# Kernel optimization log

Measured on AMD Instinct MI355X. Metric: run time of the kernel, lower is better.

Reference implementation:

```python
import jax, jax.numpy as jnp
import numpy as np

B, S, L, D, H, F, V = 8, 1024, 12, 768, 12, 3072, 21128
TITLE_LEN, CONTENTS_LEN = 64, 960
DH = D // H
NEG_INF = -1e9


def setup_inputs() -> dict:
    key = jax.random.key(0)
    ks = jax.random.split(key, 14)
    p = lambda k, shape: (0.02 * jax.random.normal(k, shape)).astype(jnp.float32)
    return {
        "x": jax.random.randint(ks[0], (B, S), 0, V),
        "y": jax.random.randint(ks[1], (B, CONTENTS_LEN), 0, V),
        "word_emb": p(ks[2], (V, D)),
        "pos_emb": p(ks[3], (S, D)),
        "type_emb": p(ks[4], (2, D)),
        "emb_ln_g": jnp.ones((D,), jnp.float32),
        "emb_ln_b": jnp.zeros((D,), jnp.float32),
        "Wq": p(ks[5], (L, D, D)), "bq": jnp.zeros((L, D), jnp.float32),
        "Wk": p(ks[6], (L, D, D)), "bk": jnp.zeros((L, D), jnp.float32),
        "Wv": p(ks[7], (L, D, D)), "bv": jnp.zeros((L, D), jnp.float32),
        "Wo": p(ks[8], (L, D, D)), "bo": jnp.zeros((L, D), jnp.float32),
        "ln1_g": jnp.ones((L, D), jnp.float32), "ln1_b": jnp.zeros((L, D), jnp.float32),
        "W1": p(ks[9], (L, D, F)), "b1": jnp.zeros((L, F), jnp.float32),
        "W2": p(ks[10], (L, F, D)), "b2": jnp.zeros((L, D), jnp.float32),
        "ln2_g": jnp.ones((L, D), jnp.float32), "ln2_b": jnp.zeros((L, D), jnp.float32),
        "cls_W": p(ks[11], (D, V)), "cls_b": jnp.zeros((V,), jnp.float32),
    }


def _ln(x, g, b):
    m = x.mean(-1, keepdims=True)
    v = jnp.mean((x - m) ** 2, -1, keepdims=True)
    return (x - m) * jax.lax.rsqrt(v + 1e-12) * g + b


def _forward(x, y, word_emb, pos_emb, type_emb, emb_ln_g, emb_ln_b,
             Wq, bq, Wk, bk, Wv, bv, Wo, bo, ln1_g, ln1_b,
             W1, b1, W2, b2, ln2_g, ln2_b, cls_W, cls_b):
    # prefix-LM mask: causal (tril) except fully-visible title block [S,S]
    mask = jnp.tril(jnp.ones((S, S), jnp.float32))
    mask = mask.at[:TITLE_LEN, :TITLE_LEN].set(1.0)
    bias = (1.0 - mask) * NEG_INF  # additive attention bias

    h = word_emb[x] + pos_emb[None, :, :] + type_emb[0]  # [B,S,D]
    h = _ln(h, emb_ln_g, emb_ln_b)

    scale = 1.0 / np.sqrt(DH).astype(np.float32)

    def step(h, p):
        Wq_, bq_, Wk_, bk_, Wv_, bv_, Wo_, bo_, g1, bb1, W1_, bf1, W2_, bf2, g2, bb2 = p
        q = (h @ Wq_ + bq_).reshape(B, S, H, DH)
        k = (h @ Wk_ + bk_).reshape(B, S, H, DH)
        v = (h @ Wv_ + bv_).reshape(B, S, H, DH)
        scores = jnp.einsum('bqhd,bkhd->bhqk', q, k) * scale + bias  # [B,H,S,S]
        a = jax.nn.softmax(scores, axis=-1)
        ctx = jnp.einsum('bhqk,bkhd->bqhd', a, v).reshape(B, S, D)
        h = _ln(h + ctx @ Wo_ + bo_, g1, bb1)
        ffn = jax.nn.gelu(h @ W1_ + bf1, approximate=False) @ W2_ + bf2
        h = _ln(h + ffn, g2, bb2)
        return h, None

    h, _ = jax.lax.scan(step, h, (Wq, bq, Wk, bk, Wv, bv, Wo, bo,
                                  ln1_g, ln1_b, W1, b1, W2, b2, ln2_g, ln2_b))

    logits = h[:, -CONTENTS_LEN:, :] @ cls_W + cls_b  # [B,C,V]
    logp = jax.nn.log_softmax(logits, axis=-1)
    valid = (y != -100)
    yc = jnp.where(valid, y, 0)
    nll = -jnp.take_along_axis(logp, yc[..., None], axis=-1)[..., 0]
    return jnp.sum(nll * valid) / jnp.maximum(jnp.sum(valid), 1)


def reference(x, y, word_emb, pos_emb, type_emb, emb_ln_g, emb_ln_b,
              Wq, bq, Wk, bk, Wv, bv, Wo, bo, ln1_g, ln1_b,
              W1, b1, W2, b2, ln2_g, ln2_b, cls_W, cls_b):
    return _forward(x, y, word_emb, pos_emb, type_emb, emb_ln_g, emb_ln_b,
                    Wq, bq, Wk, bk, Wv, bv, Wo, bo, ln1_g, ln1_b,
                    W1, b1, W2, b2, ln2_g, ln2_b, cls_W, cls_b)
```

## Files before the change

kernel.cpp:

```cpp
#include <hip/hip_runtime.h>

#define BB 8
#define SS 1024
#define LL 12
#define DD 768
#define HH 12
#define FF 3072
#define VV 21128
#define DH 64
#define CLEN 960
#define NROWS (BB * CLEN)
#define TOKS (BB * SS)
#define NQKV 2304
#define QKW 1536

typedef __attribute__((ext_vector_type(8))) short bh8;
typedef __attribute__((ext_vector_type(4))) float f32x4;
typedef __attribute__((ext_vector_type(4))) unsigned short us4;

__device__ __forceinline__ float bf2f(unsigned short u) {
    union { unsigned int i; float f; } c; c.i = ((unsigned int)u) << 16; return c.f;
}
__device__ __forceinline__ unsigned short f2bf(float f) {
    union { float f; unsigned int i; } c; c.f = f;
    unsigned int r = c.i + 0x7fffu + ((c.i >> 16) & 1u);
    return (unsigned short)(r >> 16);
}

#define GLOAD16(gsrc, ldst)                                                              \
    __builtin_amdgcn_global_load_lds((const __attribute__((address_space(1))) unsigned int*)(gsrc), \
                                     (__attribute__((address_space(3))) unsigned int*)(ldst), 16, 0, 0)

__device__ __forceinline__ float bsum256(float v, float* red) {
#pragma unroll
    for (int o = 32; o; o >>= 1) v += __shfl_down(v, o);
    if ((threadIdx.x & 63) == 0) red[threadIdx.x >> 6] = v;
    __syncthreads();
    float r = red[0] + red[1] + red[2] + red[3];
    __syncthreads();
    return r;
}

__global__ void transpose_f32_bf16(const float* __restrict__ in, unsigned short* __restrict__ out,
                                   int R, int C) {
    __shared__ float tile[32][33];
    int c0 = blockIdx.x << 5, r0 = blockIdx.y << 5;
    int tx = threadIdx.x, ty = threadIdx.y;
    for (int i = ty; i < 32; i += 8) {
        int r = r0 + i, c = c0 + tx;
        if (r < R && c < C) tile[i][tx] = in[(size_t)r * C + c];
    }
    __syncthreads();
    for (int i = ty; i < 32; i += 8) {
        int oc = c0 + i, orr = r0 + tx;
        if (oc < C && orr < R) out[(size_t)oc * R + orr] = f2bf(tile[tx][i]);
    }
}

__global__ void transpose_all(const float* __restrict__ Wq, const float* __restrict__ Wk,
                              const float* __restrict__ Wv, const float* __restrict__ Wo,
                              const float* __restrict__ W1, const float* __restrict__ W2,
                              unsigned short* __restrict__ wqkvT, unsigned short* __restrict__ woT,
                              unsigned short* __restrict__ w1T, unsigned short* __restrict__ w2T) {
    __shared__ float tile[32][33];
    int t0 = blockIdx.x;
    int l = t0 / 6912, t = t0 - l * 6912;
    const float* src;
    unsigned short* dst;
    int R, C, txt, tt;
    if (t < 1728) {
        int which = t / 576; tt = t % 576;
        src = (which == 0 ? Wq : (which == 1 ? Wk : Wv)) + (size_t)l * DD * DD;
        dst = wqkvT + (size_t)l * NQKV * DD + (size_t)which * DD * DD;
        R = DD; C = DD; txt = 24;
    } else if (t < 2304) {
        tt = t - 1728; src = Wo + (size_t)l * DD * DD; dst = woT + (size_t)l * DD * DD;
        R = DD; C = DD; txt = 24;
    } else if (t < 4608) {
        tt = t - 2304; src = W1 + (size_t)l * DD * FF; dst = w1T + (size_t)l * DD * FF;
        R = DD; C = FF; txt = 96;
    } else {
        tt = t - 4608; src = W2 + (size_t)l * FF * DD; dst = w2T + (size_t)l * FF * DD;
        R = FF; C = DD; txt = 24;
    }
    int c0 = (tt % txt) << 5, r0 = (tt / txt) << 5;
    int tx = threadIdx.x, ty = threadIdx.y;
    for (int i = ty; i < 32; i += 8) tile[i][tx] = src[(size_t)(r0 + i) * C + c0 + tx];
    __syncthreads();
    for (int i = ty; i < 32; i += 8) dst[(size_t)(c0 + i) * R + r0 + tx] = f2bf(tile[tx][i]);
}

__global__ void transpose_layer(const float* __restrict__ Wq, const float* __restrict__ Wk,
                                const float* __restrict__ Wv, const float* __restrict__ Wo,
                                const float* __restrict__ W1, const float* __restrict__ W2,
                                unsigned short* __restrict__ wqkvT, unsigned short* __restrict__ woT,
                                unsigned short* __restrict__ w1T, unsigned short* __restrict__ w2T) {
    __shared__ float tile[32][33];
    int t = blockIdx.x;
    const float* src;
    unsigned short* dst;
    int R, C, txt, tt;
    if (t < 1728) {
        int which = t / 576; tt = t % 576;
        src = which == 0 ? Wq : (which == 1 ? Wk : Wv);
        dst = wqkvT + (size_t)which * DD * DD; R = DD; C = DD; txt = 24;
    } else if (t < 2304) {
        tt = t - 1728; src = Wo; dst = woT; R = DD; C = DD; txt = 24;
    } else if (t < 4608) {
        tt = t - 2304; src = W1; dst = w1T; R = DD; C = FF; txt = 96;
    } else {
        tt = t - 4608; src = W2; dst = w2T; R = FF; C = DD; txt = 24;
    }
    int c0 = (tt % txt) << 5, r0 = (tt / txt) << 5;
    int tx = threadIdx.x, ty = threadIdx.y;
    for (int i = ty; i < 32; i += 8) tile[i][tx] = src[(size_t)(r0 + i) * C + c0 + tx];
    __syncthreads();
    for (int i = ty; i < 32; i += 8) dst[(size_t)(c0 + i) * R + r0 + tx] = f2bf(tile[tx][i]);
}

__global__ void concat_bias_all(const float* __restrict__ bq, const float* __restrict__ bk,
                                const float* __restrict__ bv, float* __restrict__ out) {
    int i = blockIdx.x * 256 + threadIdx.x;
    if (i >= LL * NQKV) return;
    int l = i / NQKV, c = i % NQKV;
    float v = c < DD ? bq[(size_t)l * DD + c]
                     : (c < 2 * DD ? bk[(size_t)l * DD + c - DD] : bv[(size_t)l * DD + c - 2 * DD]);
    out[i] = v;
}

__global__ __launch_bounds__(256) void embed_ln(const int* __restrict__ x, const float* __restrict__ we,
                                                const float* __restrict__ pe, const float* __restrict__ te,
                                                const float* __restrict__ g, const float* __restrict__ be,
                                                unsigned short* __restrict__ hb) {
    int row = blockIdx.x;
    int s = row & (SS - 1);
    int tok = x[row];
    int tid = threadIdx.x;
    __shared__ float red[4];
    float v[3];
#pragma unroll
    for (int i = 0; i < 3; i++) {
        int c = tid + i * 256;
        v[i] = we[(size_t)tok * DD + c] + pe[(size_t)s * DD + c] + te[c];
    }
    float mean = bsum256(v[0] + v[1] + v[2], red) * (1.f / DD);
    float d0 = v[0] - mean, d1 = v[1] - mean, d2 = v[2] - mean;
    float var = bsum256(d0 * d0 + d1 * d1 + d2 * d2, red) * (1.f / DD);
    float inv = rsqrtf(var + 1e-12f);
    size_t base = (size_t)row * DD;
#pragma unroll
    for (int i = 0; i < 3; i++) {
        int c = tid + i * 256;
        hb[base + c] = f2bf((v[i] - mean) * inv * g[c] + be[c]);
    }
}

__global__ __launch_bounds__(256) void add_ln(const unsigned short* __restrict__ res,
                                              const unsigned short* __restrict__ t,
                                              const float* __restrict__ g, const float* __restrict__ be,
                                              unsigned short* __restrict__ outb) {
    int row = blockIdx.x;
    int tid = threadIdx.x;
    __shared__ float red[4];
    size_t base = (size_t)row * DD;
    float v[3];
#pragma unroll
    for (int i = 0; i < 3; i++) {
        int c = tid + i * 256;
        v[i] = bf2f(res[base + c]) + bf2f(t[base + c]);
    }
    float mean = bsum256(v[0] + v[1] + v[2], red) * (1.f / DD);
    float d0 = v[0] - mean, d1 = v[1] - mean, d2 = v[2] - mean;
    float var = bsum256(d0 * d0 + d1 * d1 + d2 * d2, red) * (1.f / DD);
    float inv = rsqrtf(var + 1e-12f);
#pragma unroll
    for (int i = 0; i < 3; i++) {
        int c = tid + i * 256;
        outb[base + c] = f2bf((v[i] - mean) * inv * g[c] + be[c]);
    }
}

template <int MODE>
__global__ __launch_bounds__(256) void gemm128(const unsigned short* __restrict__ A,
                                               const unsigned short* __restrict__ BT,
                                               const float* __restrict__ bias, void* __restrict__ Cp,
                                               int M, int N, int K, int ldc, int SM,
                                               unsigned short* __restrict__ vt_out,
                                               const int* __restrict__ yv,
                                               float* __restrict__ stS, float* __restrict__ stT) {
    __shared__ __align__(16) unsigned short As[2][128 * 32];
    __shared__ __align__(16) unsigned short Bs[2][128 * 32];
    const int tid = threadIdx.x;
    const int lane = tid & 63, w = tid >> 6;
    const int fr = lane & 15, fg = lane >> 4;
    const int wr = w >> 1, wc = w & 1;

    const int Nt = gridDim.x;
    const int flat = blockIdx.y * Nt + blockIdx.x;
    const int per8 = (Nt * gridDim.y) >> 3;
    const int virt = (flat & 7) * per8 + (flat >> 3);
    const int bandSz = SM * Nt;
    const int band = virt / bandSz, rem = virt - band * bandSz;
    const int nt = rem / SM;
    const int mt = band * SM + (rem - nt * SM);
    const int m0 = mt << 7, n0 = nt << 7;

    const int srow = lane >> 2;
    const int skcol = (((lane & 3) ^ ((lane >> 3) & 3)) << 3);

    int arow0 = m0 + (w * 2 + 0) * 16 + srow;
    int arow1 = m0 + (w * 2 + 1) * 16 + srow;
    int brow0 = n0 + (w * 2 + 0) * 16 + srow;
    int brow1 = n0 + (w * 2 + 1) * 16 + srow;
    if (brow0 >= N) brow0 = N - 1;
    if (brow1 >= N) brow1 = N - 1;
    const unsigned short* aptr0 = A + (size_t)arow0 * K + skcol;
    const unsigned short* aptr1 = A + (size_t)arow1 * K + skcol;
    const unsigned short* bptr0 = BT + (size_t)brow0 * K + skcol;
    const unsigned short* bptr1 = BT + (size_t)brow1 * K + skcol;

    auto stage = [&](int bf, int k0) {
        GLOAD16(aptr0 + k0, &As[bf][(w * 2 + 0) * 512]);
        GLOAD16(aptr1 + k0, &As[bf][(w * 2 + 1) * 512]);
        GLOAD16(bptr0 + k0, &Bs[bf][(w * 2 + 0) * 512]);
        GLOAD16(bptr1 + k0, &Bs[bf][(w * 2 + 1) * 512]);
    };

    const int rdcol = ((fg ^ ((fr >> 1) & 3)) << 3);

    f32x4 acc[4][4] = {};
    stage(0, 0);
    __syncthreads();
    int cur = 0;
    for (int k0 = 0; k0 < K; k0 += 32) {
        if (k0 + 32 < K) stage(cur ^ 1, k0 + 32);
        bh8 a[4], b[4];
#pragma unroll
        for (int mi = 0; mi < 4; mi++) a[mi] = *(const bh8*)&As[cur][(wr * 64 + mi * 16 + fr) * 32 + rdcol];
#pragma unroll
        for (int ni = 0; ni < 4; ni++) b[ni] = *(const bh8*)&Bs[cur][(wc * 64 + ni * 16 + fr) * 32 + rdcol];
        __builtin_amdgcn_s_setprio(1);
#pragma unroll
        for (int mi = 0; mi < 4; mi++)
#pragma unroll
            for (int ni = 0; ni < 4; ni++)
                acc[mi][ni] = __builtin_amdgcn_mfma_f32_16x16x32_bf16(a[mi], b[ni], acc[mi][ni], 0, 0, 0);
        __builtin_amdgcn_s_setprio(0);
        __syncthreads();
        cur ^= 1;
    }

    unsigned short* Cb = (unsigned short*)Cp;
#pragma unroll
    for (int mi = 0; mi < 4; mi++) {
        int rbase = m0 + wr * 64 + mi * 16 + fg * 4;
        if (MODE == 3) {
            float e[4] = {0.f, 0.f, 0.f, 0.f};
            int yr[4];
#pragma unroll
            for (int r = 0; r < 4; r++) yr[r] = yv[rbase + r];
#pragma unroll
            for (int ni = 0; ni < 4; ni++) {
                int col = n0 + wc * 64 + ni * 16 + fr;
                if (col < N) {
                    float bb = bias[col];
#pragma unroll
                    for (int r = 0; r < 4; r++) {
                        float v = acc[mi][ni][r] + bb;
                        e[r] += __expf(v);
                        if (col == yr[r]) stT[rbase + r] = v;
                    }
                }
            }
#pragma unroll
            for (int r = 0; r < 4; r++) {
#pragma unroll
                for (int off = 1; off < 16; off <<= 1) e[r] += __shfl_xor(e[r], off);
                if (fr == 0) atomicAdd(&stS[rbase + r], e[r]);
            }
        } else {
#pragma unroll
            for (int ni = 0; ni < 4; ni++) {
                int col = n0 + wc * 64 + ni * 16 + fr;
                if (MODE == 4) {
                    float bb = bias[col];
                    if (col < 2 * DD) {
#pragma unroll
                        for (int r = 0; r < 4; r++)
                            Cb[(size_t)(rbase + r) * QKW + col] = f2bf(acc[mi][ni][r] + bb);
                    } else {
                        int g = col - 2 * DD, h = g >> 6, d = g & 63;
                        int bi = rbase >> 10, s0 = rbase & 1023;
                        us4 val;
#pragma unroll
                        for (int r = 0; r < 4; r++) val[r] = f2bf(acc[mi][ni][r] + bb);
                        *(us4*)&vt_out[(((size_t)bi * HH + h) * DH + d) * SS + s0] = val;
                    }
                } else if (col < N) {
                    float bb = bias[col];
#pragma unroll
                    for (int r = 0; r < 4; r++) {
                        float v = acc[mi][ni][r] + bb;
                        if (MODE == 2) v = 0.5f * v * (1.0f + erff(v * 0.70710678118f));
                        Cb[(size_t)(rbase + r) * ldc + col] = f2bf(v);
                    }
                }
            }
        }
    }
}

__global__ __launch_bounds__(256) void flash_attn(const unsigned short* __restrict__ qkbuf,
                                                  const unsigned short* __restrict__ VT,
                                                  unsigned short* __restrict__ ctxb) {
    const int bx = blockIdx.x;
    const int h = blockIdx.y, b = blockIdx.z;
    const int tid = threadIdx.x;
    const int lane = tid & 63, w = tid >> 6;
    const int fr = lane & 15, fg = lane >> 4;
    __shared__ unsigned short Qs[64][68];
    __shared__ unsigned short Ks[64][68];
    __shared__ unsigned short Vt[64][68];
    __shared__ unsigned short Ps[4][16][68];

    const int srow = tid >> 2, sd0 = (tid & 3) << 4;
    const unsigned short* kbase = qkbuf + (size_t)(b * SS + srow) * QKW + DD + h * 64 + sd0;
    const unsigned short* vbase = VT + (((size_t)b * HH + h) * DH + srow) * SS + sd0;

    bh8 kr0, kr1, vr0, vr1;
    auto ld_reg = [&](int kt) {
        const unsigned short* ks = kbase + (size_t)(kt * 64) * QKW;
        kr0 = *(const bh8*)ks;
        kr1 = *(const bh8*)(ks + 8);
        const unsigned short* vs = vbase + kt * 64;
        vr0 = *(const bh8*)vs;
        vr1 = *(const bh8*)(vs + 8);
    };

    for (int half = 0; half < 2; half++) {
        const int qt = (half == 0) ? 15 - bx : bx;
        __syncthreads();
        {
            const unsigned short* src = qkbuf + (size_t)(b * SS + qt * 64 + srow) * QKW + h * 64 + sd0;
            *(bh8*)&Qs[srow][sd0] = *(const bh8*)src;
            *(bh8*)&Qs[srow][sd0 + 8] = *(const bh8*)(src + 8);
        }

        f32x4 o[4] = {};
        float m[4], l[4];
#pragma unroll
        for (int r = 0; r < 4; r++) { m[r] = -3e30f; l[r] = 0.f; }

        const int nkt = (qt == 0) ? 1 : qt + 1;
        ld_reg(0);
        for (int kt = 0; kt < nkt; kt++) {
            __syncthreads();
            *(bh8*)&Ks[srow][sd0] = kr0;
            *(bh8*)&Ks[srow][sd0 + 8] = kr1;
            *(bh8*)&Vt[srow][sd0] = vr0;
            *(bh8*)&Vt[srow][sd0 + 8] = vr1;
            if (kt + 1 < nkt) ld_reg(kt + 1);
            __syncthreads();

            f32x4 s[4] = {};
            bh8 a0 = *(const bh8*)&Qs[w * 16 + fr][fg * 8];
            bh8 a1 = *(const bh8*)&Qs[w * 16 + fr][32 + fg * 8];
            __builtin_amdgcn_s_setprio(1);
#pragma unroll
            for (int cf = 0; cf < 4; cf++) {
                bh8 b0 = *(const bh8*)&Ks[cf * 16 + fr][fg * 8];
                bh8 b1 = *(const bh8*)&Ks[cf * 16 + fr][32 + fg * 8];
                s[cf] = __builtin_amdgcn_mfma_f32_16x16x32_bf16(a0, b0, s[cf], 0, 0, 0);
                s[cf] = __builtin_amdgcn_mfma_f32_16x16x32_bf16(a1, b1, s[cf], 0, 0, 0);
            }
            __builtin_amdgcn_s_setprio(0);

            const bool diag = (qt > 0) && (kt == qt);
#pragma unroll
            for (int cf = 0; cf < 4; cf++) {
#pragma unroll
                for (int r = 0; r < 4; r++) {
                    float v = s[cf][r] * 0.125f;
                    if (diag) {
                        int key = cf * 16 + fr;
                        int qrow = w * 16 + fg * 4 + r;
                        if (key > qrow) v = -1e30f;
                    }
                    s[cf][r] = v;
                }
            }
            float sc[4], mn[4];
#pragma unroll
            for (int r = 0; r < 4; r++) {
                float v = fmaxf(fmaxf(s[0][r], s[1][r]), fmaxf(s[2][r], s[3][r]));
#pragma unroll
                for (int off = 1; off < 16; off <<= 1) v = fmaxf(v, __shfl_xor(v, off));
                mn[r] = fmaxf(m[r], v);
                sc[r] = __expf(m[r] - mn[r]);
                m[r] = mn[r];
            }
#pragma unroll
            for (int cf = 0; cf < 4; cf++) {
#pragma unroll
                for (int r = 0; r < 4; r++) s[cf][r] = __expf(s[cf][r] - mn[r]);
            }
#pragma unroll
            for (int r = 0; r < 4; r++) {
                float v = s[0][r] + s[1][r] + s[2][r] + s[3][r];
#pragma unroll
                for (int off = 1; off < 16; off <<= 1) v += __shfl_xor(v, off);
                l[r] = l[r] * sc[r] + v;
            }
#pragma unroll
            for (int df = 0; df < 4; df++) {
#pragma unroll
                for (int r = 0; r < 4; r++) o[df][r] *= sc[r];
            }
#pragma unroll
            for (int cf = 0; cf < 4; cf++) {
#pragma unroll
                for (int r = 0; r < 4; r++) Ps[w][fg * 4 + r][cf * 16 + fr] = f2bf(s[cf][r]);
            }
            bh8 pa0 = *(const bh8*)&Ps[w][fr][fg * 8];
            bh8 pa1 = *(const bh8*)&Ps[w][fr][32 + fg * 8];
            __builtin_amdgcn_s_setprio(1);
#pragma unroll
            for (int df = 0; df < 4; df++) {
                bh8 vb0 = *(const bh8*)&Vt[df * 16 + fr][fg * 8];
                bh8 vb1 = *(const bh8*)&Vt[df * 16 + fr][32 + fg * 8];
                o[df] = __builtin_amdgcn_mfma_f32_16x16x32_bf16(pa0, vb0, o[df], 0, 0, 0);
                o[df] = __builtin_amdgcn_mfma_f32_16x16x32_bf16(pa1, vb1, o[df], 0, 0, 0);
            }
            __builtin_amdgcn_s_setprio(0);
        }
#pragma unroll
        for (int df = 0; df < 4; df++) {
#pragma unroll
            for (int r = 0; r < 4; r++) {
                int q = qt * 64 + w * 16 + fg * 4 + r;
                float v = o[df][r] / l[r];
                ctxb[(((size_t)b * SS + q) * HH + h) * DH + df * 16 + fr] = f2bf(v);
            }
        }
    }
}

__global__ void gather_rows(const unsigned short* __restrict__ hb, unsigned short* __restrict__ hc,
                            float* __restrict__ stS, float* __restrict__ stT) {
    int idx = blockIdx.x * 256 + threadIdx.x;
    if (idx < NROWS) { stS[idx] = 0.f; stT[idx] = 0.f; }
    if (idx >= NROWS * (DD / 8)) return;
    int g = idx / (DD / 8), c8 = (idx % (DD / 8)) * 8;
    int b = g / CLEN, cc = g % CLEN;
    *(bh8*)&hc[(size_t)g * DD + c8] = *(const bh8*)&hb[((size_t)(b * SS + 64 + cc)) * DD + c8];
}

__global__ __launch_bounds__(256) void final_reduce(const float* __restrict__ stS,
                                                    const float* __restrict__ stT, const int* __restrict__ y,
                                                    float* __restrict__ out) {
    int tid = threadIdx.x;
    float s = 0.f, c = 0.f;
    for (int i = tid; i < NROWS; i += 256) {
        if (y[i] != -100) {
            s += logf(stS[i]) - stT[i];
            c += 1.f;
        }
    }
    __shared__ float red[4];
    float gs = bsum256(s, red);
    float gc = bsum256(c, red);
    if (tid == 0) out[0] = gs / fmaxf(gc, 1.f);
}

extern "C" void kernel_launch(void* const* d_in, const int* in_sizes, int n_in,
                              void* d_out, int out_size, void* d_ws, size_t ws_size,
                              hipStream_t stream) {
    const int* x = (const int*)d_in[0];
    const int* y = (const int*)d_in[1];
    const float* we = (const float*)d_in[2];
    const float* pe = (const float*)d_in[3];
    const float* te = (const float*)d_in[4];
    const float* eg = (const float*)d_in[5];
    const float* eb = (const float*)d_in[6];
    const float* Wq = (const float*)d_in[7];
    const float* bq = (const float*)d_in[8];
    const float* Wk = (const float*)d_in[9];
    const float* bk = (const float*)d_in[10];
    const float* Wv = (const float*)d_in[11];
    const float* bv = (const float*)d_in[12];
    const float* Wo = (const float*)d_in[13];
    const float* bo = (const float*)d_in[14];
    const float* g1 = (const float*)d_in[15];
    const float* b1n = (const float*)d_in[16];
    const float* W1 = (const float*)d_in[17];
    const float* b1 = (const float*)d_in[18];
    const float* W2 = (const float*)d_in[19];
    const float* b2 = (const float*)d_in[20];
    const float* g2 = (const float*)d_in[21];
    const float* b2n = (const float*)d_in[22];
    const float* clsW = (const float*)d_in[23];
    const float* clsb = (const float*)d_in[24];
    float* out = (float*)d_out;

    char* ws = (char*)d_ws;
    size_t off = 0;
    auto alloc = [&](size_t n) {
        void* p = ws + off;
        off += n;
        off = (off + 255) & ~(size_t)255;
        return p;
    };
    unsigned short* hb   = (unsigned short*)alloc((size_t)TOKS * DD * 2);
    unsigned short* h1b  = (unsigned short*)alloc((size_t)TOKS * DD * 2);
    unsigned short* tmpb = (unsigned short*)alloc((size_t)TOKS * DD * 2);
    unsigned short* qkbuf = (unsigned short*)alloc((size_t)TOKS * QKW * 2);
    unsigned short* vtb  = (unsigned short*)alloc((size_t)TOKS * DD * 2);
    unsigned short* ctxb = (unsigned short*)alloc((size_t)TOKS * DD * 2);
    unsigned short* ffnb = (unsigned short*)alloc((size_t)TOKS * FF * 2);
    unsigned short* clsT = (unsigned short*)alloc((size_t)VV * DD * 2);
    unsigned short* hc = (unsigned short*)alloc((size_t)NROWS * DD * 2);
    float* bqkv = (float*)alloc((size_t)LL * NQKV * 4);
    float* stS = (float*)alloc(NROWS * 4);
    float* stT = (float*)alloc(NROWS * 4);

    size_t needAll = off + ((size_t)LL * (NQKV + DD + FF + FF) * DD * 2) + 4096;
    const bool bigWs = ws_size >= needAll;
    const int WL = bigWs ? LL : 1;
    unsigned short* wqkvT = (unsigned short*)alloc((size_t)WL * NQKV * DD * 2);
    unsigned short* woT = (unsigned short*)alloc((size_t)WL * DD * DD * 2);
    unsigned short* w1T = (unsigned short*)alloc((size_t)WL * DD * FF * 2);
    unsigned short* w2T = (unsigned short*)alloc((size_t)WL * DD * FF * 2);

    dim3 tb(32, 8);
    transpose_f32_bf16<<<dim3((VV + 31) / 32, DD / 32), tb, 0, stream>>>(clsW, clsT, DD, VV);
    concat_bias_all<<<(LL * NQKV + 255) / 256, 256, 0, stream>>>(bq, bk, bv, bqkv);
    if (bigWs)
        transpose_all<<<LL * 6912, tb, 0, stream>>>(Wq, Wk, Wv, Wo, W1, W2, wqkvT, woT, w1T, w2T);
    embed_ln<<<TOKS, 256, 0, stream>>>(x, we, pe, te, eg, eb, hb);

    for (int l = 0; l < LL; l++) {
        const int wl = bigWs ? l : 0;
        if (!bigWs)
            transpose_layer<<<6912, tb, 0, stream>>>(Wq + (size_t)l * DD * DD, Wk + (size_t)l * DD * DD,
                                                     Wv + (size_t)l * DD * DD, Wo + (size_t)l * DD * DD,
                                                     W1 + (size_t)l * DD * FF, W2 + (size_t)l * FF * DD,
                                                     wqkvT, woT, w1T, w2T);

        gemm128<4><<<dim3(NQKV / 128, TOKS / 128), 256, 0, stream>>>(
            hb, wqkvT + (size_t)wl * NQKV * DD, bqkv + (size_t)l * NQKV,
            qkbuf, TOKS, NQKV, DD, NQKV, 8, vtb, nullptr, nullptr, nullptr);

        flash_attn<<<dim3(8, HH, BB), 256, 0, stream>>>(qkbuf, vtb, ctxb);

        gemm128<1><<<dim3(DD / 128, TOKS / 128), 256, 0, stream>>>(
            ctxb, woT + (size_t)wl * DD * DD, bo + (size_t)l * DD, tmpb,
            TOKS, DD, DD, DD, 8, nullptr, nullptr, nullptr, nullptr);
        add_ln<<<TOKS, 256, 0, stream>>>(hb, tmpb, g1 + (size_t)l * DD, b1n + (size_t)l * DD, h1b);

        gemm128<2><<<dim3(FF / 128, TOKS / 128), 256, 0, stream>>>(
            h1b, w1T + (size_t)wl * DD * FF, b1 + (size_t)l * FF, ffnb,
            TOKS, FF, DD, FF, 8, nullptr, nullptr, nullptr, nullptr);
        gemm128<1><<<dim3(DD / 128, TOKS / 128), 256, 0, stream>>>(
            ffnb, w2T + (size_t)wl * DD * FF, b2 + (size_t)l * DD, tmpb,
            TOKS, DD, FF, DD, 8, nullptr, nullptr, nullptr, nullptr);
        add_ln<<<TOKS, 256, 0, stream>>>(h1b, tmpb, g2 + (size_t)l * DD, b2n + (size_t)l * DD, hb);
    }

    gather_rows<<<(NROWS * (DD / 8) + 255) / 256, 256, 0, stream>>>(hb, hc, stS, stT);
    gemm128<3><<<dim3((VV + 127) / 128, NROWS / 128), 256, 0, stream>>>(hc, clsT, clsb, nullptr,
                                                                        NROWS, VV, DD, VV, 6, nullptr,
                                                                        y, stS, stT);
    final_reduce<<<1, 256, 0, stream>>>(stS, stT, y, out);
}
```

Measured before the change: 4.213 ms.

## Double-buffer K/V tiles in flash attention and drop GEMM LDS swizzle

Flash attention now keeps two LDS buffers for K and V. The next tile is written to the spare buffer after the current tile's PV MFMAs, which removes one of the two barriers per key tile. Separately, the GEMM drops its XOR swizzle on LDS stage and read columns and uses plain fg*8 offsets. Without the swizzle the 32-element-wide rows are likely to cause LDS bank conflicts, and the extra K/V buffers raise flash attention's LDS use.

```diff
diff --git a/kernel.cpp b/kernel.cpp
--- a/kernel.cpp
+++ b/kernel.cpp
@@ -206,7 +206,7 @@
     const int m0 = mt << 7, n0 = nt << 7;
 
     const int srow = lane >> 2;
-    const int skcol = (((lane & 3) ^ ((lane >> 3) & 3)) << 3);
+    const int skcol = (lane & 3) << 3;
 
     int arow0 = m0 + (w * 2 + 0) * 16 + srow;
     int arow1 = m0 + (w * 2 + 1) * 16 + srow;
@@ -226,8 +226,6 @@
         GLOAD16(bptr1 + k0, &Bs[bf][(w * 2 + 1) * 512]);
     };
 
-    const int rdcol = ((fg ^ ((fr >> 1) & 3)) << 3);
-
     f32x4 acc[4][4] = {};
     stage(0, 0);
     __syncthreads();
@@ -236,9 +234,9 @@
         if (k0 + 32 < K) stage(cur ^ 1, k0 + 32);
         bh8 a[4], b[4];
 #pragma unroll
-        for (int mi = 0; mi < 4; mi++) a[mi] = *(const bh8*)&As[cur][(wr * 64 + mi * 16 + fr) * 32 + rdcol];
-#pragma unroll
-        for (int ni = 0; ni < 4; ni++) b[ni] = *(const bh8*)&Bs[cur][(wc * 64 + ni * 16 + fr) * 32 + rdcol];
+        for (int mi = 0; mi < 4; mi++) a[mi] = *(const bh8*)&As[cur][(wr * 64 + mi * 16 + fr) * 32 + fg * 8];
+#pragma unroll
+        for (int ni = 0; ni < 4; ni++) b[ni] = *(const bh8*)&Bs[cur][(wc * 64 + ni * 16 + fr) * 32 + fg * 8];
         __builtin_amdgcn_s_setprio(1);
 #pragma unroll
         for (int mi = 0; mi < 4; mi++)
@@ -319,8 +317,8 @@
     const int lane = tid & 63, w = tid >> 6;
     const int fr = lane & 15, fg = lane >> 4;
     __shared__ unsigned short Qs[64][68];
-    __shared__ unsigned short Ks[64][68];
-    __shared__ unsigned short Vt[64][68];
+    __shared__ unsigned short Ks[2][64][68];
+    __shared__ unsigned short Vt[2][64][68];
     __shared__ unsigned short Ps[4][16][68];
 
     const int srow = tid >> 2, sd0 = (tid & 3) << 4;
@@ -339,37 +337,36 @@
 
     for (int half = 0; half < 2; half++) {
         const int qt = (half == 0) ? 15 - bx : bx;
+        const int nkt = (qt == 0) ? 1 : qt + 1;
         __syncthreads();
         {
             const unsigned short* src = qkbuf + (size_t)(b * SS + qt * 64 + srow) * QKW + h * 64 + sd0;
             *(bh8*)&Qs[srow][sd0] = *(const bh8*)src;
             *(bh8*)&Qs[srow][sd0 + 8] = *(const bh8*)(src + 8);
         }
+        ld_reg(0);
+        *(bh8*)&Ks[0][srow][sd0] = kr0;
+        *(bh8*)&Ks[0][srow][sd0 + 8] = kr1;
+        *(bh8*)&Vt[0][srow][sd0] = vr0;
+        *(bh8*)&Vt[0][srow][sd0 + 8] = vr1;
+        if (nkt > 1) ld_reg(1);
+        __syncthreads();
 
         f32x4 o[4] = {};
         float m[4], l[4];
 #pragma unroll
         for (int r = 0; r < 4; r++) { m[r] = -3e30f; l[r] = 0.f; }
 
-        const int nkt = (qt == 0) ? 1 : qt + 1;
-        ld_reg(0);
+        int cur = 0;
         for (int kt = 0; kt < nkt; kt++) {
-            __syncthreads();
-            *(bh8*)&Ks[srow][sd0] = kr0;
-            *(bh8*)&Ks[srow][sd0 + 8] = kr1;
-            *(bh8*)&Vt[srow][sd0] = vr0;
-            *(bh8*)&Vt[srow][sd0 + 8] = vr1;
-            if (kt + 1 < nkt) ld_reg(kt + 1);
-            __syncthreads();
-
             f32x4 s[4] = {};
             bh8 a0 = *(const bh8*)&Qs[w * 16 + fr][fg * 8];
             bh8 a1 = *(const bh8*)&Qs[w * 16 + fr][32 + fg * 8];
             __builtin_amdgcn_s_setprio(1);
 #pragma unroll
             for (int cf = 0; cf < 4; cf++) {
-                bh8 b0 = *(const bh8*)&Ks[cf * 16 + fr][fg * 8];
-                bh8 b1 = *(const bh8*)&Ks[cf * 16 + fr][32 + fg * 8];
+                bh8 b0 = *(const bh8*)&Ks[cur][cf * 16 + fr][fg * 8];
+                bh8 b1 = *(const bh8*)&Ks[cur][cf * 16 + fr][32 + fg * 8];
                 s[cf] = __builtin_amdgcn_mfma_f32_16x16x32_bf16(a0, b0, s[cf], 0, 0, 0);
                 s[cf] = __builtin_amdgcn_mfma_f32_16x16x32_bf16(a1, b1, s[cf], 0, 0, 0);
             }
@@ -426,12 +423,22 @@
             __builtin_amdgcn_s_setprio(1);
 #pragma unroll
             for (int df = 0; df < 4; df++) {
-                bh8 vb0 = *(const bh8*)&Vt[df * 16 + fr][fg * 8];
-                bh8 vb1 = *(const bh8*)&Vt[df * 16 + fr][32 + fg * 8];
+                bh8 vb0 = *(const bh8*)&Vt[cur][df * 16 + fr][fg * 8];
+                bh8 vb1 = *(const bh8*)&Vt[cur][df * 16 + fr][32 + fg * 8];
                 o[df] = __builtin_amdgcn_mfma_f32_16x16x32_bf16(pa0, vb0, o[df], 0, 0, 0);
                 o[df] = __builtin_amdgcn_mfma_f32_16x16x32_bf16(pa1, vb1, o[df], 0, 0, 0);
             }
             __builtin_amdgcn_s_setprio(0);
+
+            if (kt + 1 < nkt) {
+                *(bh8*)&Ks[cur ^ 1][srow][sd0] = kr0;
+                *(bh8*)&Ks[cur ^ 1][srow][sd0 + 8] = kr1;
+                *(bh8*)&Vt[cur ^ 1][srow][sd0] = vr0;
+                *(bh8*)&Vt[cur ^ 1][srow][sd0 + 8] = vr1;
+                if (kt + 2 < nkt) ld_reg(kt + 2);
+            }
+            __syncthreads();
+            cur ^= 1;
         }
 #pragma unroll
         for (int df = 0; df < 4; df++) {
```

After: 4.263 ms. Within noise of the previous version (+1.2%).
